# Performance work log

Measured on AMD Instinct MI355X. Metric: run time of the kernel, lower is better.

## Reference

```python
import jax, jax.numpy as jnp
import numpy as np

N, E, R, B, DIN, H1, H2 = 50000, 1000000, 8, 30, 64, 64, 64


def setup_inputs() -> dict:
    key = jax.random.key(0)
    ks = jax.random.split(key, 12)
    node_features = jax.random.normal(ks[0], (N, DIN), dtype=jnp.float32)
    src = jax.random.randint(ks[1], (E,), 0, N)
    dst = jax.random.randint(ks[2], (E,), 0, N)
    edge_index = jnp.stack([src, dst]).astype(jnp.int64)
    edge_norm = jax.random.uniform(ks[3], (E,), dtype=jnp.float32)
    edge_type = jax.random.randint(ks[4], (E,), 0, R).astype(jnp.int64)
    s = 0.05  # param init scale
    basis = jax.random.normal(ks[5], (B, DIN, H1), dtype=jnp.float32) * s
    comp = jax.random.normal(ks[6], (R, B), dtype=jnp.float32) * s
    loop_weight = jax.random.normal(ks[7], (DIN, H1), dtype=jnp.float32) * s
    bias1 = jnp.zeros((H1,), dtype=jnp.float32)
    weight2 = jax.random.normal(ks[8], (H1, H2), dtype=jnp.float32) * s
    bias2 = jnp.zeros((H2,), dtype=jnp.float32)
    return dict(node_features=node_features, edge_index=edge_index,
                edge_norm=edge_norm, edge_type=edge_type, basis=basis,
                comp=comp, loop_weight=loop_weight, bias1=bias1,
                weight2=weight2, bias2=bias2)


def reference(node_features, edge_index, edge_norm, edge_type, basis, comp,
              loop_weight, bias1, weight2, bias2):
    n = node_features.shape[0]
    src, dst = edge_index[0], edge_index[1]

    # ---- RGCNConv (basis decomposition, sum aggregation, self-loop, bias) ----
    # relation weights from bases: [R, DIN, H1]
    Wrel = jnp.einsum('rb,bio->rio', comp, basis)
    # transform every node by every relation once: [N, R, H1]
    xr = jnp.einsum('ni,rio->nro', node_features, Wrel)
    # per-edge message via (src, edge_type) gather: [E, H1]
    msg = xr[src, edge_type]
    agg1 = jax.ops.segment_sum(msg, dst, num_segments=n)
    h = agg1 + node_features @ loop_weight + bias1

    # ---- GraphConv (symmetric 'both' normalization) ----
    ones = jnp.ones((src.shape[0],), dtype=h.dtype)
    deg_out = jnp.clip(jax.ops.segment_sum(ones, src, num_segments=n), 1.0, None)
    deg_in = jnp.clip(jax.ops.segment_sum(ones, dst, num_segments=n), 1.0, None)
    hs = h * jax.lax.rsqrt(deg_out)[:, None]
    agg2 = jax.ops.segment_sum(hs[src], dst, num_segments=n)
    agg2 = agg2 * jax.lax.rsqrt(deg_in)[:, None]
    out = agg2 @ weight2 + bias2
    return out
```

## Files before the change

kernel.cpp:

```cpp
#include <hip/hip_runtime.h>

#define N_NODES 50000
#define N_EDGES 1000000
#define NB      128
#define CHUNK   7813
#define NQ      8
#define QN      6256
#define NBLK2   196

#define A_PART    0
#define A_XR      0
#define A_DEGP    115200000
#define A_ROWPTR  115400000
#define A_BSUM    115600128
#define A_BBASE   115601024
#define A_CSR     115601920
#define A_HS      123601920
#define A_WALL    136401920

typedef unsigned int uint32;

__global__ void k_wall(const float* __restrict__ comp, const float* __restrict__ basis,
                       const float* __restrict__ loopw, float* __restrict__ Wall) {
    int idx = blockIdx.x * 256 + threadIdx.x;
    if (idx >= 9 * 4096) return;
    int r = idx >> 12, io = idx & 4095;
    float acc;
    if (r < 8) {
        acc = 0.f;
        #pragma unroll
        for (int b = 0; b < 30; ++b) acc += comp[r * 30 + b] * basis[b * 4096 + io];
    } else {
        acc = loopw[io];
    }
    Wall[idx] = acc;
}

__global__ __launch_bounds__(256) void k_hist2(const int* __restrict__ ei,
                                               uint32* __restrict__ part) {
    __shared__ __align__(16) uint32 h[QN];
    int t = threadIdx.x, b = blockIdx.x, q = blockIdx.y;
    int lo = q * QN;
    int nq = N_NODES - lo; if (nq > QN) nq = QN;
    int4* h4 = (int4*)h;
    for (int i = t; i < QN / 4; i += 256) h4[i] = make_int4(0, 0, 0, 0);
    __syncthreads();
    int e0 = b * CHUNK, e1 = e0 + CHUNK;
    if (e1 > N_EDGES) e1 = N_EDGES;
    for (int e = e0 + t; e < e1; e += 256) {
        int s = ei[e], d = ei[N_EDGES + e];
        unsigned rs = (unsigned)(s - lo), rd = (unsigned)(d - lo);
        if (rs < (unsigned)QN) atomicAdd(&h[rs], 1u);
        if (rd < (unsigned)QN) atomicAdd(&h[rd], 0x10000u);
    }
    __syncthreads();
    int4* d4 = (int4*)(part + b * N_NODES + lo);
    const int4* s4 = (const int4*)h;
    for (int i = t; i < nq / 4; i += 256) d4[i] = s4[i];
}

__global__ __launch_bounds__(256) void k_merge(const uint32* __restrict__ part,
                                               uint32* __restrict__ degp,
                                               int* __restrict__ bsum) {
    int t = threadIdx.x, v = blockIdx.x * 256 + t;
    uint32 s = 0;
    if (v < N_NODES) {
        #pragma unroll 8
        for (int b = 0; b < NB; ++b) s += part[b * N_NODES + v];
        degp[v] = s;
    }
    int din = (int)(s >> 16);
    int r = din;
    #pragma unroll
    for (int d = 1; d < 64; d <<= 1) r += __shfl_xor(r, d);
    __shared__ int wsum[4];
    int lane = t & 63, wid = t >> 6;
    if (lane == 0) wsum[wid] = r;
    __syncthreads();
    if (t == 0) bsum[blockIdx.x] = wsum[0] + wsum[1] + wsum[2] + wsum[3];
}

__global__ void k_scanb(const int* __restrict__ bsum, int* __restrict__ bbase) {
    int t = threadIdx.x;
    int v = (t < NBLK2) ? bsum[t] : 0;
    int lane = t & 63, wid = t >> 6;
    int x = v;
    #pragma unroll
    for (int d = 1; d < 64; d <<= 1) {
        int y = __shfl_up(x, d);
        if (lane >= d) x += y;
    }
    __shared__ int wsum[4];
    if (lane == 63) wsum[wid] = x;
    __syncthreads();
    int base = 0;
    for (int w = 0; w < wid; ++w) base += wsum[w];
    if (t < NBLK2) bbase[t] = base + x - v;
}

__global__ __launch_bounds__(256) void k_base(uint32* __restrict__ part,
                                              const uint32* __restrict__ degp,
                                              const int* __restrict__ bbase,
                                              int* __restrict__ rowptr) {
    int t = threadIdx.x, v = blockIdx.x * 256 + t;
    int din = (v < N_NODES) ? (int)(degp[v] >> 16) : 0;
    int lane = t & 63, wid = t >> 6;
    int x = din;
    #pragma unroll
    for (int d = 1; d < 64; d <<= 1) {
        int y = __shfl_up(x, d);
        if (lane >= d) x += y;
    }
    __shared__ int wsum[4];
    if (lane == 63) wsum[wid] = x;
    __syncthreads();
    int base = bbase[blockIdx.x];
    for (int w = 0; w < wid; ++w) base += wsum[w];
    int start = base + x - din;
    if (v < N_NODES) {
        rowptr[v] = start;
        if (v == N_NODES - 1) rowptr[N_NODES] = start + din;
        uint32 run = (uint32)start;
        for (int b = 0; b < NB; ++b) {
            uint32 p = part[b * N_NODES + v];
            part[b * N_NODES + v] = run;
            run += (p >> 16);
        }
    }
}

__global__ __launch_bounds__(256) void k_fill2(const int* __restrict__ ei,
                                               const int* __restrict__ etype,
                                               const uint32* __restrict__ fillbase,
                                               int2* __restrict__ csr) {
    __shared__ __align__(16) uint32 cur[QN];
    int t = threadIdx.x, b = blockIdx.x, q = blockIdx.y;
    int lo = q * QN;
    int nq = N_NODES - lo; if (nq > QN) nq = QN;
    const int4* s4 = (const int4*)(fillbase + b * N_NODES + lo);
    int4* c4 = (int4*)cur;
    for (int i = t; i < nq / 4; i += 256) c4[i] = s4[i];
    __syncthreads();
    int e0 = b * CHUNK, e1 = e0 + CHUNK;
    if (e1 > N_EDGES) e1 = N_EDGES;
    for (int e = e0 + t; e < e1; e += 256) {
        int d = ei[N_EDGES + e];
        unsigned rd = (unsigned)(d - lo);
        if (rd < (unsigned)QN) {
            int s = ei[e], ty = etype[e];
            uint32 pos = atomicAdd(&cur[rd], 1u);
            csr[pos] = make_int2(s * 9 + ty, s);
        }
    }
}

__global__ __launch_bounds__(256) void k_xr(const float* __restrict__ x,
                                            const float* __restrict__ Wall,
                                            float* __restrict__ xr) {
    __shared__ __align__(16) float At[32 * 256];
    __shared__ __align__(16) float Wt[32 * 64];
    int t = threadIdx.x;
    int n0 = blockIdx.x * 256;
    int r = blockIdx.y;
    int og = t & 7, ng = t >> 3;
    float acc[8][8];
    #pragma unroll
    for (int i = 0; i < 8; ++i)
        #pragma unroll
        for (int j = 0; j < 8; ++j) acc[i][j] = 0.f;

    #pragma unroll
    for (int ph = 0; ph < 2; ++ph) {
        if (ph) __syncthreads();
        #pragma unroll
        for (int j = 0; j < 8; ++j) {
            int f4 = t + j * 256;
            int n = f4 >> 3, k4 = f4 & 7;
            float4 v = make_float4(0.f, 0.f, 0.f, 0.f);
            if (n0 + n < N_NODES)
                v = *(const float4*)&x[(n0 + n) * 64 + ph * 32 + k4 * 4];
            int sl = n >> 2, nl = n & 3, kb = k4 * 4;
            At[(kb + 0) * 256 + (((sl ^ ((kb + 0) & 7)) << 2) | nl)] = v.x;
            At[(kb + 1) * 256 + (((sl ^ ((kb + 1) & 7)) << 2) | nl)] = v.y;
            At[(kb + 2) * 256 + (((sl ^ ((kb + 2) & 7)) << 2) | nl)] = v.z;
            At[(kb + 3) * 256 + (((sl ^ ((kb + 3) & 7)) << 2) | nl)] = v.w;
        }
        #pragma unroll
        for (int j = 0; j < 8; ++j) {
            int f = t + j * 256;
            Wt[f] = Wall[r * 4096 + ph * 2048 + f];
        }
        __syncthreads();
        #pragma unroll 4
        for (int k = 0; k < 32; ++k) {
            int c = k & 7;
            float4 aA = *(const float4*)&At[k * 256 + (((2 * ng) ^ c) << 2)];
            float4 aB = *(const float4*)&At[k * 256 + (((2 * ng + 1) ^ c) << 2)];
            float4 w0 = *(const float4*)&Wt[k * 64 + og * 8];
            float4 w1 = *(const float4*)&Wt[k * 64 + og * 8 + 4];
            float a_[8] = {aA.x, aA.y, aA.z, aA.w, aB.x, aB.y, aB.z, aB.w};
            float w_[8] = {w0.x, w0.y, w0.z, w0.w, w1.x, w1.y, w1.z, w1.w};
            #pragma unroll
            for (int i = 0; i < 8; ++i)
                #pragma unroll
                for (int j = 0; j < 8; ++j) acc[i][j] += a_[i] * w_[j];
        }
    }
    #pragma unroll
    for (int i = 0; i < 8; ++i) {
        int n = n0 + ng * 8 + i;
        if (n < N_NODES) {
            *(float4*)&xr[n * 576 + r * 64 + og * 8] =
                make_float4(acc[i][0], acc[i][1], acc[i][2], acc[i][3]);
            *(float4*)&xr[n * 576 + r * 64 + og * 8 + 4] =
                make_float4(acc[i][4], acc[i][5], acc[i][6], acc[i][7]);
        }
    }
}

__global__ __launch_bounds__(256) void k_agg1(const float* __restrict__ xr,
                                              const int2* __restrict__ csr,
                                              const int* __restrict__ rowptr,
                                              const uint32* __restrict__ degp,
                                              const float* __restrict__ bias1,
                                              float* __restrict__ hs) {
    int wid = threadIdx.x >> 6, lane = threadIdx.x & 63;
    int v = blockIdx.x * 4 + wid;
    if (v >= N_NODES) return;
    float acc = xr[(v * 9 + 8) * 64 + lane] + bias1[lane];
    int j = rowptr[v], end = rowptr[v + 1];
    for (; j + 4 <= end; j += 4) {
        int r0 = csr[j].x, r1 = csr[j + 1].x, r2 = csr[j + 2].x, r3 = csr[j + 3].x;
        float a0 = xr[r0 * 64 + lane], a1 = xr[r1 * 64 + lane];
        float a2 = xr[r2 * 64 + lane], a3 = xr[r3 * 64 + lane];
        acc += a0; acc += a1; acc += a2; acc += a3;
    }
    for (; j < end; ++j) acc += xr[csr[j].x * 64 + lane];
    float dg = (float)(degp[v] & 0xffffu);
    if (dg < 1.f) dg = 1.f;
    hs[v * 64 + lane] = acc * rsqrtf(dg);
}

__global__ __launch_bounds__(256) void k_layer2(const float* __restrict__ hs,
                                                const int2* __restrict__ csr,
                                                const int* __restrict__ rowptr,
                                                const uint32* __restrict__ degp,
                                                const float* __restrict__ w2,
                                                const float* __restrict__ bias2,
                                                float* __restrict__ out) {
    __shared__ __align__(16) float W2s[64 * 64];
    __shared__ __align__(16) float ys[4 * 64];
    int t = threadIdx.x;
    #pragma unroll
    for (int j = 0; j < 16; ++j) W2s[t + j * 256] = w2[t + j * 256];
    int wid = t >> 6, lane = t & 63;
    int v = blockIdx.x * 4 + wid;
    float acc = 0.f;
    int j = 0, end = 0;
    if (v < N_NODES) { j = rowptr[v]; end = rowptr[v + 1]; }
    for (; j + 4 <= end; j += 4) {
        int r0 = csr[j].y, r1 = csr[j + 1].y, r2 = csr[j + 2].y, r3 = csr[j + 3].y;
        float a0 = hs[r0 * 64 + lane], a1 = hs[r1 * 64 + lane];
        float a2 = hs[r2 * 64 + lane], a3 = hs[r3 * 64 + lane];
        acc += a0; acc += a1; acc += a2; acc += a3;
    }
    for (; j < end; ++j) acc += hs[csr[j].y * 64 + lane];
    if (v < N_NODES) {
        float dg = (float)(degp[v] >> 16);
        if (dg < 1.f) dg = 1.f;
        ys[wid * 64 + lane] = acc * rsqrtf(dg);
    }
    __syncthreads();
    if (v >= N_NODES) return;
    float o = bias2[lane];
    const float* yrow = &ys[wid * 64];
    #pragma unroll 4
    for (int k = 0; k < 64; ++k) o += yrow[k] * W2s[k * 64 + lane];
    out[v * 64 + lane] = o;
}

extern "C" void kernel_launch(void* const* d_in, const int* in_sizes, int n_in,
                              void* d_out, int out_size, void* d_ws, size_t ws_size,
                              hipStream_t stream) {
    const float* x      = (const float*)d_in[0];
    const int*   ei     = (const int*)d_in[1];
    const int*   etype  = (const int*)d_in[3];
    const float* basis  = (const float*)d_in[4];
    const float* comp   = (const float*)d_in[5];
    const float* loopw  = (const float*)d_in[6];
    const float* bias1  = (const float*)d_in[7];
    const float* w2     = (const float*)d_in[8];
    const float* bias2  = (const float*)d_in[9];
    float* out = (float*)d_out;

    char* ws = (char*)d_ws;
    uint32* part   = (uint32*)(ws + A_PART);
    float*  xr     = (float*)(ws + A_XR);
    uint32* degp   = (uint32*)(ws + A_DEGP);
    int*    rowptr = (int*)(ws + A_ROWPTR);
    int*    bsum   = (int*)(ws + A_BSUM);
    int*    bbase  = (int*)(ws + A_BBASE);
    int2*   csr    = (int2*)(ws + A_CSR);
    float*  hs     = (float*)(ws + A_HS);
    float*  Wall   = (float*)(ws + A_WALL);

    k_wall<<<144, 256, 0, stream>>>(comp, basis, loopw, Wall);
    k_hist2<<<dim3(NB, NQ), 256, 0, stream>>>(ei, part);
    k_merge<<<NBLK2, 256, 0, stream>>>(part, degp, bsum);
    k_scanb<<<1, 256, 0, stream>>>(bsum, bbase);
    k_base<<<NBLK2, 256, 0, stream>>>(part, degp, bbase, rowptr);
    k_fill2<<<dim3(NB, NQ), 256, 0, stream>>>(ei, etype, part, csr);
    k_xr<<<dim3((N_NODES + 255) / 256, 9), 256, 0, stream>>>(x, Wall, xr);
    k_agg1<<<N_NODES / 4, 256, 0, stream>>>(xr, csr, rowptr, degp, bias1, hs);
    k_layer2<<<N_NODES / 4, 256, 0, stream>>>(hs, csr, rowptr, degp, w2, bias2, out);
}
```

Before: 310.2 us.

## Restructure xr GEMM to wave-uniform weight loads and halve binning blocks

The per-relation node transform kernel drops the shared-memory weight tile. Each wave now owns 16 output columns, read with wave-uniform (readfirstlane-indexed) global loads that can become scalar loads, while each lane computes 4 nodes from a wider XOR-swizzled A tile. This removes one LDS staging pass and cuts LDS traffic for the weights. The output stores change shape, each lane writing a 4-node by 16-column block. Separately, the edge-binning kernels use 64 blocks with twice-larger chunks instead of 128, which cuts per-block overhead but lowers parallelism.

After: 351.9 us. 1.13x slower.

```diff
diff --git a/kernel.cpp b/kernel.cpp
--- a/kernel.cpp
+++ b/kernel.cpp
@@ -2,8 +2,8 @@
 
 #define N_NODES 50000
 #define N_EDGES 1000000
-#define NB      128
-#define CHUNK   7813
+#define NB      64
+#define CHUNK   15625
 #define NQ      8
 #define QN      6256
 #define NBLK2   196
@@ -158,18 +158,18 @@
                                             const float* __restrict__ Wall,
                                             float* __restrict__ xr) {
     __shared__ __align__(16) float At[32 * 256];
-    __shared__ __align__(16) float Wt[32 * 64];
     int t = threadIdx.x;
     int n0 = blockIdx.x * 256;
     int r = blockIdx.y;
-    int og = t & 7, ng = t >> 3;
-    float acc[8][8];
-    #pragma unroll
-    for (int i = 0; i < 8; ++i)
+    int w = __builtin_amdgcn_readfirstlane(t >> 6);
+    int l = t & 63;
+    const float* __restrict__ Wr = Wall + r * 4096 + w * 16;
+    float acc[4][16];
+    #pragma unroll
+    for (int i = 0; i < 4; ++i)
         #pragma unroll
-        for (int j = 0; j < 8; ++j) acc[i][j] = 0.f;
-
-    #pragma unroll
+        for (int j = 0; j < 16; ++j) acc[i][j] = 0.f;
+
     for (int ph = 0; ph < 2; ++ph) {
         if (ph) __syncthreads();
         #pragma unroll
@@ -180,40 +180,38 @@
             if (n0 + n < N_NODES)
                 v = *(const float4*)&x[(n0 + n) * 64 + ph * 32 + k4 * 4];
             int sl = n >> 2, nl = n & 3, kb = k4 * 4;
-            At[(kb + 0) * 256 + (((sl ^ ((kb + 0) & 7)) << 2) | nl)] = v.x;
-            At[(kb + 1) * 256 + (((sl ^ ((kb + 1) & 7)) << 2) | nl)] = v.y;
-            At[(kb + 2) * 256 + (((sl ^ ((kb + 2) & 7)) << 2) | nl)] = v.z;
-            At[(kb + 3) * 256 + (((sl ^ ((kb + 3) & 7)) << 2) | nl)] = v.w;
-        }
+            At[(kb + 0) * 256 + (((sl ^ (kb + 0)) & 63) << 2) + nl] = v.x;
+            At[(kb + 1) * 256 + (((sl ^ (kb + 1)) & 63) << 2) + nl] = v.y;
+            At[(kb + 2) * 256 + (((sl ^ (kb + 2)) & 63) << 2) + nl] = v.z;
+            At[(kb + 3) * 256 + (((sl ^ (kb + 3)) & 63) << 2) + nl] = v.w;
+        }
+        __syncthreads();
+        const float* __restrict__ Wp = Wr + ph * 32 * 64;
         #pragma unroll
-        for (int j = 0; j < 8; ++j) {
-            int f = t + j * 256;
-            Wt[f] = Wall[r * 4096 + ph * 2048 + f];
-        }
-        __syncthreads();
-        #pragma unroll 4
         for (int k = 0; k < 32; ++k) {
-            int c = k & 7;
-            float4 aA = *(const float4*)&At[k * 256 + (((2 * ng) ^ c) << 2)];
-            float4 aB = *(const float4*)&At[k * 256 + (((2 * ng + 1) ^ c) << 2)];
-            float4 w0 = *(const float4*)&Wt[k * 64 + og * 8];
-            float4 w1 = *(const float4*)&Wt[k * 64 + og * 8 + 4];
-            float a_[8] = {aA.x, aA.y, aA.z, aA.w, aB.x, aB.y, aB.z, aB.w};
-            float w_[8] = {w0.x, w0.y, w0.z, w0.w, w1.x, w1.y, w1.z, w1.w};
+            float4 a = *(const float4*)&At[k * 256 + (((l ^ k) & 63) << 2)];
+            float4 w0 = *(const float4*)&Wp[k * 64 + 0];
+            float4 w1 = *(const float4*)&Wp[k * 64 + 4];
+            float4 w2 = *(const float4*)&Wp[k * 64 + 8];
+            float4 w3 = *(const float4*)&Wp[k * 64 + 12];
+            float a_[4] = {a.x, a.y, a.z, a.w};
+            float w_[16] = {w0.x, w0.y, w0.z, w0.w, w1.x, w1.y, w1.z, w1.w,
+                            w2.x, w2.y, w2.z, w2.w, w3.x, w3.y, w3.z, w3.w};
             #pragma unroll
-            for (int i = 0; i < 8; ++i)
+            for (int i = 0; i < 4; ++i)
                 #pragma unroll
-                for (int j = 0; j < 8; ++j) acc[i][j] += a_[i] * w_[j];
-        }
-    }
-    #pragma unroll
-    for (int i = 0; i < 8; ++i) {
-        int n = n0 + ng * 8 + i;
+                for (int j = 0; j < 16; ++j) acc[i][j] += a_[i] * w_[j];
+        }
+    }
+    #pragma unroll
+    for (int i = 0; i < 4; ++i) {
+        int n = n0 + l * 4 + i;
         if (n < N_NODES) {
-            *(float4*)&xr[n * 576 + r * 64 + og * 8] =
-                make_float4(acc[i][0], acc[i][1], acc[i][2], acc[i][3]);
-            *(float4*)&xr[n * 576 + r * 64 + og * 8 + 4] =
-                make_float4(acc[i][4], acc[i][5], acc[i][6], acc[i][7]);
+            float* dst = &xr[n * 576 + r * 64 + w * 16];
+            *(float4*)&dst[0]  = make_float4(acc[i][0],  acc[i][1],  acc[i][2],  acc[i][3]);
+            *(float4*)&dst[4]  = make_float4(acc[i][4],  acc[i][5],  acc[i][6],  acc[i][7]);
+            *(float4*)&dst[8]  = make_float4(acc[i][8],  acc[i][9],  acc[i][10], acc[i][11]);
+            *(float4*)&dst[12] = make_float4(acc[i][12], acc[i][13], acc[i][14], acc[i][15]);
         }
     }
 }
```

## Split layer-2 into aggregation kernel and register-tiled GEMM kernel

Applied to the files above, without the earlier changes.

Layer 2 was a fused kernel in which every 4-node block reloaded the full 64x64 W2 into shared memory and ran a per-lane dot product. It is now split into a pure gather-aggregate kernel that writes normalized rows to a workspace buffer reusing the xr region, followed by a register-tiled 256x64 GEMM with swizzled shared-memory tiles. This removes the redundant per-block W2 loads and the low-reuse matmul. The cost is an extra launch and a round trip of the 12.8 MB intermediate through global memory.

New measurement: 310.1 us. Within noise of the previous version (-0.0%).

```diff
diff --git a/kernel.cpp b/kernel.cpp
--- a/kernel.cpp
+++ b/kernel.cpp
@@ -10,6 +10,7 @@
 
 #define A_PART    0
 #define A_XR      0
+#define A_Y2      0
 #define A_DEGP    115200000
 #define A_ROWPTR  115400000
 #define A_BSUM    115600128
@@ -241,23 +242,16 @@
     hs[v * 64 + lane] = acc * rsqrtf(dg);
 }
 
-__global__ __launch_bounds__(256) void k_layer2(const float* __restrict__ hs,
-                                                const int2* __restrict__ csr,
-                                                const int* __restrict__ rowptr,
-                                                const uint32* __restrict__ degp,
-                                                const float* __restrict__ w2,
-                                                const float* __restrict__ bias2,
-                                                float* __restrict__ out) {
-    __shared__ __align__(16) float W2s[64 * 64];
-    __shared__ __align__(16) float ys[4 * 64];
-    int t = threadIdx.x;
-    #pragma unroll
-    for (int j = 0; j < 16; ++j) W2s[t + j * 256] = w2[t + j * 256];
-    int wid = t >> 6, lane = t & 63;
+__global__ __launch_bounds__(256) void k_agg2(const float* __restrict__ hs,
+                                              const int2* __restrict__ csr,
+                                              const int* __restrict__ rowptr,
+                                              const uint32* __restrict__ degp,
+                                              float* __restrict__ y2) {
+    int wid = threadIdx.x >> 6, lane = threadIdx.x & 63;
     int v = blockIdx.x * 4 + wid;
+    if (v >= N_NODES) return;
     float acc = 0.f;
-    int j = 0, end = 0;
-    if (v < N_NODES) { j = rowptr[v]; end = rowptr[v + 1]; }
+    int j = rowptr[v], end = rowptr[v + 1];
     for (; j + 4 <= end; j += 4) {
         int r0 = csr[j].y, r1 = csr[j + 1].y, r2 = csr[j + 2].y, r3 = csr[j + 3].y;
         float a0 = hs[r0 * 64 + lane], a1 = hs[r1 * 64 + lane];
@@ -265,18 +259,77 @@
         acc += a0; acc += a1; acc += a2; acc += a3;
     }
     for (; j < end; ++j) acc += hs[csr[j].y * 64 + lane];
-    if (v < N_NODES) {
-        float dg = (float)(degp[v] >> 16);
-        if (dg < 1.f) dg = 1.f;
-        ys[wid * 64 + lane] = acc * rsqrtf(dg);
-    }
-    __syncthreads();
-    if (v >= N_NODES) return;
-    float o = bias2[lane];
-    const float* yrow = &ys[wid * 64];
-    #pragma unroll 4
-    for (int k = 0; k < 64; ++k) o += yrow[k] * W2s[k * 64 + lane];
-    out[v * 64 + lane] = o;
+    float dg = (float)(degp[v] >> 16);
+    if (dg < 1.f) dg = 1.f;
+    y2[v * 64 + lane] = acc * rsqrtf(dg);
+}
+
+__global__ __launch_bounds__(256) void k_gemm2(const float* __restrict__ y2,
+                                               const float* __restrict__ w2,
+                                               const float* __restrict__ bias2,
+                                               float* __restrict__ out) {
+    __shared__ __align__(16) float At[32 * 256];
+    __shared__ __align__(16) float Wt[32 * 64];
+    int t = threadIdx.x;
+    int n0 = blockIdx.x * 256;
+    int og = t & 7, ng = t >> 3;
+    float acc[8][8];
+    #pragma unroll
+    for (int i = 0; i < 8; ++i)
+        #pragma unroll
+        for (int j = 0; j < 8; ++j) acc[i][j] = 0.f;
+
+    #pragma unroll
+    for (int ph = 0; ph < 2; ++ph) {
+        if (ph) __syncthreads();
+        #pragma unroll
+        for (int j = 0; j < 8; ++j) {
+            int f4 = t + j * 256;
+            int n = f4 >> 3, k4 = f4 & 7;
+            float4 v = make_float4(0.f, 0.f, 0.f, 0.f);
+            if (n0 + n < N_NODES)
+                v = *(const float4*)&y2[(n0 + n) * 64 + ph * 32 + k4 * 4];
+            int sl = n >> 2, nl = n & 3, kb = k4 * 4;
+            At[(kb + 0) * 256 + (((sl ^ ((kb + 0) & 7)) << 2) | nl)] = v.x;
+            At[(kb + 1) * 256 + (((sl ^ ((kb + 1) & 7)) << 2) | nl)] = v.y;
+            At[(kb + 2) * 256 + (((sl ^ ((kb + 2) & 7)) << 2) | nl)] = v.z;
+            At[(kb + 3) * 256 + (((sl ^ ((kb + 3) & 7)) << 2) | nl)] = v.w;
+        }
+        #pragma unroll
+        for (int j = 0; j < 8; ++j) {
+            int f = t + j * 256;
+            Wt[f] = w2[ph * 2048 + f];
+        }
+        __syncthreads();
+        #pragma unroll 4
+        for (int k = 0; k < 32; ++k) {
+            int c = k & 7;
+            float4 aA = *(const float4*)&At[k * 256 + (((2 * ng) ^ c) << 2)];
+            float4 aB = *(const float4*)&At[k * 256 + (((2 * ng + 1) ^ c) << 2)];
+            float4 w0 = *(const float4*)&Wt[k * 64 + og * 8];
+            float4 w1 = *(const float4*)&Wt[k * 64 + og * 8 + 4];
+            float a_[8] = {aA.x, aA.y, aA.z, aA.w, aB.x, aB.y, aB.z, aB.w};
+            float w_[8] = {w0.x, w0.y, w0.z, w0.w, w1.x, w1.y, w1.z, w1.w};
+            #pragma unroll
+            for (int i = 0; i < 8; ++i)
+                #pragma unroll
+                for (int j = 0; j < 8; ++j) acc[i][j] += a_[i] * w_[j];
+        }
+    }
+    float4 b0 = *(const float4*)&bias2[og * 8];
+    float4 b1 = *(const float4*)&bias2[og * 8 + 4];
+    #pragma unroll
+    for (int i = 0; i < 8; ++i) {
+        int n = n0 + ng * 8 + i;
+        if (n < N_NODES) {
+            *(float4*)&out[n * 64 + og * 8] =
+                make_float4(acc[i][0] + b0.x, acc[i][1] + b0.y,
+                            acc[i][2] + b0.z, acc[i][3] + b0.w);
+            *(float4*)&out[n * 64 + og * 8 + 4] =
+                make_float4(acc[i][4] + b1.x, acc[i][5] + b1.y,
+                            acc[i][6] + b1.z, acc[i][7] + b1.w);
+        }
+    }
 }
 
 extern "C" void kernel_launch(void* const* d_in, const int* in_sizes, int n_in,
@@ -296,6 +349,7 @@
     char* ws = (char*)d_ws;
     uint32* part   = (uint32*)(ws + A_PART);
     float*  xr     = (float*)(ws + A_XR);
+    float*  y2     = (float*)(ws + A_Y2);
     uint32* degp   = (uint32*)(ws + A_DEGP);
     int*    rowptr = (int*)(ws + A_ROWPTR);
     int*    bsum   = (int*)(ws + A_BSUM);
@@ -312,5 +366,6 @@
     k_fill2<<<dim3(NB, NQ), 256, 0, stream>>>(ei, etype, part, csr);
     k_xr<<<dim3((N_NODES + 255) / 256, 9), 256, 0, stream>>>(x, Wall, xr);
     k_agg1<<<N_NODES / 4, 256, 0, stream>>>(xr, csr, rowptr, degp, bias1, hs);
-    k_layer2<<<N_NODES / 4, 256, 0, stream>>>(hs, csr, rowptr, degp, w2, bias2, out);
-}
+    k_agg2<<<N_NODES / 4, 256, 0, stream>>>(hs, csr, rowptr, degp, y2);
+    k_gemm2<<<(N_NODES + 255) / 256, 256, 0, stream>>>(y2, w2, bias2, out);
+}
```
